# Kernel optimization log

Hardware: AMD Instinct MI355X
Metric: run time of the kernel (lower is better)

The kernel has to match this reference:

```python
import jax, jax.numpy as jnp
import numpy as np
import math

G = 256        # graphs per batch
N = 2048       # nodes per graph (uniform)
D = 128        # dim_in
E = 4194304    # edges (avg degree 8)
DE = 16        # edge_attr dim
RATIO = 0.5    # cfg.gnn.pool_ratio


def setup_inputs() -> dict:
    key = jax.random.key(0)
    k1, k2, k3, k4 = jax.random.split(key, 4)
    x = jax.random.normal(k1, (G * N, D), jnp.float32)
    edge_index = jax.random.randint(k2, (2, E), 0, G * N, jnp.int32)
    edge_attr = jax.random.normal(k3, (E, DE), jnp.float32)
    batch = jnp.repeat(jnp.arange(G, dtype=jnp.int32), N)
    weight = jax.random.normal(k4, (D,), jnp.float32)  # TopKPooling score projection
    return {"x": x, "edge_index": edge_index, "edge_attr": edge_attr,
            "batch": batch, "weight": weight, "num_graphs": G}


def reference(x, edge_index, edge_attr, batch, weight, num_graphs):
    n_total = x.shape[0]
    n = n_total // num_graphs              # uniform nodes per graph
    k = int(math.ceil(RATIO * n))          # nodes kept per graph (static)

    # PyG TopKPooling score: tanh((x . w) / ||w||)
    score = jnp.tanh((x @ weight) / jnp.linalg.norm(weight))  # [n_total]

    # per-graph top-k (uniform graph sizes -> reshape + lax.top_k)
    top_idx = jax.lax.top_k(score.reshape(num_graphs, n), k)[1]          # [G, k]
    offs = (jnp.arange(num_graphs, dtype=top_idx.dtype) * n)[:, None]
    perm = (top_idx + offs).reshape(-1)                                  # [G*k] global node ids

    # gate kept node features by their score
    x_out = x[perm] * score[perm][:, None]                               # [G*k, D]
    batch_out = jnp.repeat(jnp.arange(num_graphs, dtype=batch.dtype), k)

    # filter_adj: remap kept nodes to new ids, drop edges touching removed nodes
    new_ids = jnp.arange(perm.shape[0], dtype=jnp.int32)
    node_map = jnp.full((n_total,), -1, jnp.int32).at[perm].set(new_ids)
    ns = node_map[edge_index[0]]
    nd = node_map[edge_index[1]]
    edge_mask = (ns >= 0) & (nd >= 0)                                    # [E]
    edge_index_out = jnp.where(edge_mask, jnp.stack([ns, nd]), -1)       # [2, E], -1 = dropped
    edge_attr_out = jnp.where(edge_mask[:, None], edge_attr, 0.0)        # [E, DE]

    return x_out, edge_index_out, edge_attr_out, batch_out, edge_mask
```

## Files before the change

### kernel.cpp

```cpp
#include <hip/hip_runtime.h>


typedef float f32x4_v __attribute__((ext_vector_type(4)));

__device__ inline void nt_store4(float4 v, float4* p) {
  f32x4_v t; t.x = v.x; t.y = v.y; t.z = v.z; t.w = v.w;
  __builtin_nontemporal_store(t, reinterpret_cast<f32x4_v*>(p));
}
__device__ inline float4 nt_load4(const float4* p) {
  f32x4_v t = __builtin_nontemporal_load(reinterpret_cast<const f32x4_v*>(p));
  return make_float4(t.x, t.y, t.z, t.w);
}

#define TK_PAD(j) ((j) + ((j) >> 4))

__global__ __launch_bounds__(1024) void score_topk_kernel(
    const float* __restrict__ x, const float* __restrict__ w,
    float* __restrict__ gate, int* __restrict__ perm,
    int* __restrict__ node_map, int n, int k) {
  __shared__ unsigned long long skey[2048 + 128];
  __shared__ int sidx[2048 + 128];
  const int g = blockIdx.x;
  const int tid = threadIdx.x;

  {
    int l = tid & 63;
    float2 wv2 = reinterpret_cast<const float2*>(w)[l];
    float wsq = wv2.x * wv2.x + wv2.y * wv2.y;
#pragma unroll
    for (int off = 32; off > 0; off >>= 1) wsq += __shfl_xor(wsq, off);
    float inv = __frsqrt_rn(wsq);

    const int grp = tid >> 4;
    const int sub = tid & 15;
    const float4* wp = reinterpret_cast<const float4*>(w + sub * 8);
    const float4 wa = wp[0], wb = wp[1];
    const float* xg = x + (size_t)g * n * 128;

#pragma unroll 2
    for (int r0 = grp; r0 < n; r0 += 64) {
      const float4* xp =
          reinterpret_cast<const float4*>(xg + (size_t)r0 * 128 + sub * 8);
      float4 a = xp[0], b = xp[1];
      double dot = (double)a.x * wa.x + (double)a.y * wa.y +
                   (double)a.z * wa.z + (double)a.w * wa.w +
                   (double)b.x * wb.x + (double)b.y * wb.y +
                   (double)b.z * wb.z + (double)b.w * wb.w;
#pragma unroll
      for (int off = 8; off > 0; off >>= 1) dot += __shfl_xor(dot, off);
      if (sub == 0) {
        unsigned long long bb = (unsigned long long)__double_as_longlong(dot);
        unsigned long long u =
            (bb & 0x8000000000000000ULL) ? ~bb : (bb | 0x8000000000000000ULL);
        skey[TK_PAD(r0)] = ~u;
        sidx[TK_PAD(r0)] = r0;
        gate[g * n + r0] = tanhf((float)dot * inv);
      }
    }
  }

  for (int size = 2; size <= n; size <<= 1) {
    for (int stride = size >> 1; stride > 0; stride >>= 1) {
      __syncthreads();
      int lo = ((tid & ~(stride - 1)) << 1) | (tid & (stride - 1));
      int hi = lo + stride;
      bool asc = ((lo & size) == 0);
      int plo = TK_PAD(lo), phi = TK_PAD(hi);
      unsigned long long ka = skey[plo], kb = skey[phi];
      int ia = sidx[plo], ib = sidx[phi];
      bool hi_lt_lo = (kb < ka) || (kb == ka && ib < ia);
      bool lo_lt_hi = (ka < kb) || (ka == kb && ia < ib);
      if (asc ? hi_lt_lo : lo_lt_hi) {
        skey[plo] = kb; skey[phi] = ka;
        sidx[plo] = ib; sidx[phi] = ia;
      }
    }
  }
  __syncthreads();

  for (int r = tid; r < n; r += 1024) {
    int node = g * n + sidx[TK_PAD(r)];
    node_map[node] = (r < k) ? (g * k + r) : -1;
    if (r < k) perm[g * k + r] = node;
  }
}

__global__ __launch_bounds__(256) void output_kernel(
    const float* __restrict__ x, const float* __restrict__ gate,
    const int* __restrict__ perm, const int* __restrict__ node_map,
    const int* __restrict__ edge_index, const float4* __restrict__ attr,
    float* __restrict__ x_out, float* __restrict__ batch_out,
    float* __restrict__ eio, float* __restrict__ mask_out,
    float4* __restrict__ attr_out, int E, int k, int NB_G) {
  const int bid = (int)blockIdx.x;
  if (bid < NB_G) {
    int d4 = threadIdx.x & 31;
    int rbase = bid * 32 + ((int)threadIdx.x >> 5);
#pragma unroll
    for (int r4 = 0; r4 < 4; ++r4) {
      int row = rbase + r4 * 8;
      int src = perm[row];
      float s = gate[src];
      float4 v = *reinterpret_cast<const float4*>(x + (size_t)src * 128 + d4 * 4);
      v.x *= s; v.y *= s; v.z *= s; v.w *= s;
      nt_store4(v, reinterpret_cast<float4*>(x_out + (size_t)row * 128 + d4 * 4));
      if (d4 == 0)
        __builtin_nontemporal_store((float)(row / k), batch_out + row);
    }
  } else {
    __shared__ float smask[256];
    const int ebase = (bid - NB_G) * 512;
    for (int it = 0; it < 2; ++it) {
      int e = ebase + it * 256 + (int)threadIdx.x;
      int s0 = __builtin_nontemporal_load(edge_index + e);
      int s1 = __builtin_nontemporal_load(edge_index + E + e);
      int ns = node_map[s0];
      int nd = node_map[s1];
      bool m = (ns >= 0) && (nd >= 0);
      float z = m ? 1.0f : 0.0f;
      __builtin_nontemporal_store(m ? (float)ns : -1.0f, eio + e);
      __builtin_nontemporal_store(m ? (float)nd : -1.0f, eio + E + e);
      __builtin_nontemporal_store(z, mask_out + e);
      smask[threadIdx.x] = z;
      __syncthreads();
      const float4* ablk = attr + (size_t)(ebase + it * 256) * 4;
      float4* oblk = attr_out + (size_t)(ebase + it * 256) * 4;
#pragma unroll
      for (int j = 0; j < 4; ++j) {
        int idx = j * 256 + (int)threadIdx.x;
        float zz = smask[idx >> 2];
        float4 a = nt_load4(ablk + idx);
        a.x *= zz; a.y *= zz; a.z *= zz; a.w *= zz;
        nt_store4(a, oblk + idx);
      }
      __syncthreads();
    }
  }
}

extern "C" void kernel_launch(void* const* d_in, const int* in_sizes, int n_in,
                              void* d_out, int out_size, void* d_ws, size_t ws_size,
                              hipStream_t stream) {
  const float* x          = (const float*)d_in[0];
  const int*   edge_index = (const int*)d_in[1];
  const float* edge_attr  = (const float*)d_in[2];
  const float* w          = (const float*)d_in[4];

  const int D = 128;
  const int n_total = in_sizes[0] / D;
  const int E = in_sizes[1] / 2;
  const int G = 256;
  const int n = n_total / G;
  const int k = (n + 1) / 2;
  const int total_rows = G * k;

  float* out       = (float*)d_out;
  float* x_out     = out;
  float* eio       = x_out + (size_t)total_rows * D;
  float* attr_out  = eio + (size_t)2 * E;
  float* batch_out = attr_out + (size_t)E * 16;
  float* mask_out  = batch_out + total_rows;

  float* gate   = (float*)d_ws;
  int* perm     = (int*)(gate + n_total);
  int* node_map = perm + total_rows;

  score_topk_kernel<<<G, 1024, 0, stream>>>(x, w, gate, perm, node_map, n, k);

  const int NB_G = total_rows / 32;
  const int NB_E = E / 512;
  output_kernel<<<NB_G + NB_E, 256, 0, stream>>>(
      x, gate, perm, node_map, edge_index, (const float4*)edge_attr,
      x_out, batch_out, eio, mask_out, (float4*)attr_out, E, k, NB_G);
}
```

Measured before the change: 225.2 us.

## Fuse gated row gather into top-k kernel, keep gate and perm in LDS

After: 222.3 us. About the same (-1.3%).

```diff
diff --git a/kernel.cpp b/kernel.cpp
--- a/kernel.cpp
+++ b/kernel.cpp
@@ -14,14 +14,16 @@
 
 #define TK_PAD(j) ((j) + ((j) >> 4))
 
-__global__ __launch_bounds__(1024) void score_topk_kernel(
+__global__ __launch_bounds__(1024) void score_topk_gather_kernel(
     const float* __restrict__ x, const float* __restrict__ w,
-    float* __restrict__ gate, int* __restrict__ perm,
-    int* __restrict__ node_map, int n, int k) {
+    int* __restrict__ node_map, float* __restrict__ x_out,
+    float* __restrict__ batch_out, int n, int k) {
   __shared__ unsigned long long skey[2048 + 128];
   __shared__ int sidx[2048 + 128];
+  __shared__ float gate_lds[2048];
   const int g = blockIdx.x;
   const int tid = threadIdx.x;
+  const float* xg = x + (size_t)g * n * 128;
 
   {
     int l = tid & 63;
@@ -35,7 +37,6 @@
     const int sub = tid & 15;
     const float4* wp = reinterpret_cast<const float4*>(w + sub * 8);
     const float4 wa = wp[0], wb = wp[1];
-    const float* xg = x + (size_t)g * n * 128;
 
 #pragma unroll 2
     for (int r0 = grp; r0 < n; r0 += 64) {
@@ -54,7 +55,7 @@
             (bb & 0x8000000000000000ULL) ? ~bb : (bb | 0x8000000000000000ULL);
         skey[TK_PAD(r0)] = ~u;
         sidx[TK_PAD(r0)] = r0;
-        gate[g * n + r0] = tanhf((float)dot * inv);
+        gate_lds[r0] = tanhf((float)dot * inv);
       }
     }
   }
@@ -79,62 +80,55 @@
   __syncthreads();
 
   for (int r = tid; r < n; r += 1024) {
-    int node = g * n + sidx[TK_PAD(r)];
-    node_map[node] = (r < k) ? (g * k + r) : -1;
-    if (r < k) perm[g * k + r] = node;
+    int sl = sidx[TK_PAD(r)];
+    node_map[g * n + sl] = (r < k) ? (g * k + r) : -1;
+    if (r < k) __builtin_nontemporal_store((float)g, batch_out + g * k + r);
+  }
+
+  const int d4 = tid & 31;
+  const int rr = tid >> 5;
+  float* xo = x_out + (size_t)g * k * 128;
+#pragma unroll 2
+  for (int it = 0; it < 32; ++it) {
+    int r = it * 32 + rr;
+    int sl = sidx[TK_PAD(r)];
+    float s = gate_lds[sl];
+    float4 v = *reinterpret_cast<const float4*>(xg + (size_t)sl * 128 + d4 * 4);
+    v.x *= s; v.y *= s; v.z *= s; v.w *= s;
+    nt_store4(v, reinterpret_cast<float4*>(xo + (size_t)r * 128 + d4 * 4));
   }
 }
 
-__global__ __launch_bounds__(256) void output_kernel(
-    const float* __restrict__ x, const float* __restrict__ gate,
-    const int* __restrict__ perm, const int* __restrict__ node_map,
-    const int* __restrict__ edge_index, const float4* __restrict__ attr,
-    float* __restrict__ x_out, float* __restrict__ batch_out,
-    float* __restrict__ eio, float* __restrict__ mask_out,
-    float4* __restrict__ attr_out, int E, int k, int NB_G) {
-  const int bid = (int)blockIdx.x;
-  if (bid < NB_G) {
-    int d4 = threadIdx.x & 31;
-    int rbase = bid * 32 + ((int)threadIdx.x >> 5);
+__global__ __launch_bounds__(256) void edge_kernel(
+    const int* __restrict__ edge_index, const int* __restrict__ node_map,
+    const float4* __restrict__ attr, float* __restrict__ eio,
+    float* __restrict__ mask_out, float4* __restrict__ attr_out, int E) {
+  __shared__ float smask[256];
+  const int ebase = (int)blockIdx.x * 512;
+  for (int it = 0; it < 2; ++it) {
+    int e = ebase + it * 256 + (int)threadIdx.x;
+    int s0 = __builtin_nontemporal_load(edge_index + e);
+    int s1 = __builtin_nontemporal_load(edge_index + E + e);
+    int ns = node_map[s0];
+    int nd = node_map[s1];
+    bool m = (ns >= 0) && (nd >= 0);
+    float z = m ? 1.0f : 0.0f;
+    __builtin_nontemporal_store(m ? (float)ns : -1.0f, eio + e);
+    __builtin_nontemporal_store(m ? (float)nd : -1.0f, eio + E + e);
+    __builtin_nontemporal_store(z, mask_out + e);
+    smask[threadIdx.x] = z;
+    __syncthreads();
+    const float4* ablk = attr + (size_t)(ebase + it * 256) * 4;
+    float4* oblk = attr_out + (size_t)(ebase + it * 256) * 4;
 #pragma unroll
-    for (int r4 = 0; r4 < 4; ++r4) {
-      int row = rbase + r4 * 8;
-      int src = perm[row];
-      float s = gate[src];
-      float4 v = *reinterpret_cast<const float4*>(x + (size_t)src * 128 + d4 * 4);
-      v.x *= s; v.y *= s; v.z *= s; v.w *= s;
-      nt_store4(v, reinterpret_cast<float4*>(x_out + (size_t)row * 128 + d4 * 4));
-      if (d4 == 0)
-        __builtin_nontemporal_store((float)(row / k), batch_out + row);
+    for (int j = 0; j < 4; ++j) {
+      int idx = j * 256 + (int)threadIdx.x;
+      float zz = smask[idx >> 2];
+      float4 a = nt_load4(ablk + idx);
+      a.x *= zz; a.y *= zz; a.z *= zz; a.w *= zz;
+      nt_store4(a, oblk + idx);
     }
-  } else {
-    __shared__ float smask[256];
-    const int ebase = (bid - NB_G) * 512;
-    for (int it = 0; it < 2; ++it) {
-      int e = ebase + it * 256 + (int)threadIdx.x;
-      int s0 = __builtin_nontemporal_load(edge_index + e);
-      int s1 = __builtin_nontemporal_load(edge_index + E + e);
-      int ns = node_map[s0];
-      int nd = node_map[s1];
-      bool m = (ns >= 0) && (nd >= 0);
-      float z = m ? 1.0f : 0.0f;
-      __builtin_nontemporal_store(m ? (float)ns : -1.0f, eio + e);
-      __builtin_nontemporal_store(m ? (float)nd : -1.0f, eio + E + e);
-      __builtin_nontemporal_store(z, mask_out + e);
-      smask[threadIdx.x] = z;
-      __syncthreads();
-      const float4* ablk = attr + (size_t)(ebase + it * 256) * 4;
-      float4* oblk = attr_out + (size_t)(ebase + it * 256) * 4;
-#pragma unroll
-      for (int j = 0; j < 4; ++j) {
-        int idx = j * 256 + (int)threadIdx.x;
-        float zz = smask[idx >> 2];
-        float4 a = nt_load4(ablk + idx);
-        a.x *= zz; a.y *= zz; a.z *= zz; a.w *= zz;
-        nt_store4(a, oblk + idx);
-      }
-      __syncthreads();
-    }
+    __syncthreads();
   }
 }
 
@@ -161,15 +155,11 @@
   float* batch_out = attr_out + (size_t)E * 16;
   float* mask_out  = batch_out + total_rows;
 
-  float* gate   = (float*)d_ws;
-  int* perm     = (int*)(gate + n_total);
-  int* node_map = perm + total_rows;
+  int* node_map = (int*)d_ws;
 
-  score_topk_kernel<<<G, 1024, 0, stream>>>(x, w, gate, perm, node_map, n, k);
-
-  const int NB_G = total_rows / 32;
-  const int NB_E = E / 512;
-  output_kernel<<<NB_G + NB_E, 256, 0, stream>>>(
-      x, gate, perm, node_map, edge_index, (const float4*)edge_attr,
-      x_out, batch_out, eio, mask_out, (float4*)attr_out, E, k, NB_G);
+  score_topk_gather_kernel<<<G, 1024, 0, stream>>>(
+      x, w, node_map, x_out, batch_out, n, k);
+  edge_kernel<<<E / 512, 256, 0, stream>>>(
+      edge_index, node_map, (const float4*)edge_attr, eio, mask_out,
+      (float4*)attr_out, E);
 }
```
